# Optimization experiments

Hardware: AMD Instinct MI355X
Metric: run time of the kernel (lower is better)

The kernel has to match this reference:

```python
import jax, jax.numpy as jnp
import numpy as np
from jax import lax

TOP_K = 500
NEG_SLOPE = 0.01  # nn.LeakyReLU default
MASK_VAL = -10000.0


def setup_inputs() -> dict:
    key = jax.random.key(0)
    ks = jax.random.split(key, 6)
    B, N, D, H, C = 256, 131072, 2048, 512, 4096
    return {
        "inputs": jax.random.normal(ks[0], (B, D), dtype=jnp.float32),
        "targets": jax.random.randint(ks[1], (B,), 0, C, dtype=jnp.int32),
        "sample_features": jax.random.normal(ks[2], (N, D), dtype=jnp.float32),
        "sample_labels": jax.random.randint(ks[3], (N,), 0, C, dtype=jnp.int32),
        "fc1_w": jax.random.normal(ks[4], (D, H), dtype=jnp.float32) * (1.0 / np.sqrt(D)),
        "fc1_b": jnp.zeros((H,), dtype=jnp.float32),
        "fc2_w": jax.random.normal(ks[5], (H, 1), dtype=jnp.float32) * (1.0 / np.sqrt(H)),
        "fc2_b": jnp.zeros((1,), dtype=jnp.float32),
    }


def _head(d, w1, b1, w2, b2):
    h = jax.nn.leaky_relu(d @ w1 + b1, negative_slope=NEG_SLOPE)
    return h @ w2 + b2  # [B, 1] logits


def reference(inputs, targets, sample_features, sample_labels, fc1_w, fc1_b, fc2_w, fc2_b):
    B = inputs.shape[0]
    x = inputs / jnp.linalg.norm(inputs, axis=1, keepdims=True)  # F.normalize
    # similarities against memory bank: [B, N]
    sims = x @ sample_features.T
    pos_mask = sample_labels[None, :] == targets[:, None]  # [B, N]
    masked = jnp.where(pos_mask, MASK_VAL, sims)  # temp_sims[k, pos] = -10000
    # top-500 most-similar non-positive bank entries per row (sort()[1][-500:])
    _, top_idx = lax.top_k(masked, TOP_K)  # [B, 500]
    # stand-in for python random.choice (deterministic jax randomness)
    key = jax.random.key(42)
    k_neg, k_pos = jax.random.split(key)
    neg_pick = jax.random.randint(k_neg, (B,), 0, TOP_K)
    neg_sel = jnp.take_along_axis(top_idx, neg_pick[:, None], axis=1)[:, 0]  # [B]
    # uniform random positive via gumbel-argmax over the positive mask
    g = jax.random.gumbel(k_pos, pos_mask.shape, dtype=jnp.float32)
    pos_sel = jnp.argmax(jnp.where(pos_mask, g, -jnp.inf), axis=1)  # [B]
    x2_neg = sample_features[neg_sel]  # [B, D]
    x2_pos = sample_features[pos_sel]  # [B, D]
    logit_neg = _head(jnp.abs(x - x2_neg), fc1_w, fc1_b, fc2_w, fc2_b)
    logit_pos = _head(jnp.abs(x - x2_pos), fc1_w, fc1_b, fc2_w, fc2_b)
    # BCEWithLogits: y=1 -> softplus(-x); y=0 -> softplus(x); mean reduction
    loss_positive = jnp.mean(jax.nn.softplus(-logit_pos))
    loss_negtive = jnp.mean(jax.nn.softplus(logit_neg))
    loss_siamese = loss_positive + loss_negtive
    return loss_siamese
```

## Files before the change

kernel.cpp:

```cpp
#include <hip/hip_runtime.h>
#include <hip/hip_bf16.h>
#include <stdint.h>

#define N_BANK 131072
#define B_ROWS 256
#define DIM 2048
#define HID 512
#define CAND_CAP 1024
#define WIN 64
#define Z_THRESH 2.5528f

typedef __attribute__((ext_vector_type(8))) short bf16x8;
typedef __attribute__((ext_vector_type(8))) unsigned short ushort8;
typedef __attribute__((ext_vector_type(4))) float f32x4;

__device__ __forceinline__ void threefry2x32(uint32_t k0, uint32_t k1,
                                             uint32_t x0, uint32_t x1,
                                             uint32_t& o0, uint32_t& o1) {
  uint32_t ks0 = k0, ks1 = k1, ks2 = k0 ^ k1 ^ 0x1BD11BDAu;
  uint32_t ks[3] = {ks0, ks1, ks2};
  x0 += ks0; x1 += ks1;
  const int rotA[4] = {13, 15, 26, 6};
  const int rotB[4] = {17, 29, 16, 24};
  #pragma unroll
  for (int g = 0; g < 5; ++g) {
    const int* rr = (g & 1) ? rotB : rotA;
    #pragma unroll
    for (int i = 0; i < 4; ++i) {
      x0 += x1;
      x1 = (x1 << rr[i]) | (x1 >> (32 - rr[i]));
      x1 ^= x0;
    }
    x0 += ks[(g + 1) % 3];
    x1 += ks[(g + 2) % 3] + (uint32_t)(g + 1);
  }
  o0 = x0; o1 = x1;
}

__device__ __forceinline__ void jax_split(uint32_t k0, uint32_t k1,
                                          uint32_t& a0, uint32_t& a1,
                                          uint32_t& b0, uint32_t& b1) {
  uint32_t o00, o10, o01, o11;
  threefry2x32(k0, k1, 0u, 2u, o00, o10);
  threefry2x32(k0, k1, 1u, 3u, o01, o11);
  a0 = o00; a1 = o01;
  b0 = o10; b1 = o11;
}

__device__ __forceinline__ ushort f2bf(float f) {
  uint32_t u = __float_as_uint(f);
  return (ushort)((u + 0x7FFFu + ((u >> 16) & 1u)) >> 16);
}

__device__ __forceinline__ uint32_t cvt_pk(float lo, float hi) {
  uint32_t d;
  asm("v_cvt_pk_bf16_f32 %0, %1, %2" : "=v"(d) : "v"(lo), "v"(hi));
  return d;
}

__device__ __forceinline__ bf16x8 cvt8(float4 a, float4 b) {
  union { uint32_t u[4]; bf16x8 v; } r;
  r.u[0] = cvt_pk(a.x, a.y);
  r.u[1] = cvt_pk(a.z, a.w);
  r.u[2] = cvt_pk(b.x, b.y);
  r.u[3] = cvt_pk(b.z, b.w);
  return r.v;
}

__device__ __forceinline__ void async16(const void* g, void* l) {
  __builtin_amdgcn_global_load_lds((const __attribute__((address_space(1))) void*)g,
                                   (__attribute__((address_space(3))) void*)l, 16, 0, 0);
}

__global__ void zero_kernel(int* __restrict__ cand_cnt,
                            unsigned long long* __restrict__ pos_comb) {
  int t = threadIdx.x;
  cand_cnt[t] = 0;
  pos_comb[t] = 0ull;
}

__global__ __launch_bounds__(256) void prep_pos(const float* __restrict__ inputs,
                                                ushort* __restrict__ Abf,
                                                float* __restrict__ invn,
                                                float* __restrict__ thr,
                                                const int* __restrict__ labels,
                                                const int* __restrict__ targets,
                                                unsigned long long* __restrict__ pos_comb) {
  int bid = blockIdx.x, t = threadIdx.x;
  __shared__ int targ_s[256];
  __shared__ uint32_t bm[128];
  __shared__ double red[256];
  if (t < 128) bm[t] = 0u;
  int tg = targets[t];
  targ_s[t] = tg;

  double s = 0.0;
  if (bid < 256) {
    const float* src = inputs + (size_t)bid * DIM + t * 8;
    float4 v0 = *(const float4*)(src);
    float4 v1 = *(const float4*)(src + 4);
    s = (double)v0.x * v0.x + (double)v0.y * v0.y + (double)v0.z * v0.z + (double)v0.w * v0.w
      + (double)v1.x * v1.x + (double)v1.y * v1.y + (double)v1.z * v1.z + (double)v1.w * v1.w;
    ushort8 c = { f2bf(v0.x), f2bf(v0.y), f2bf(v0.z), f2bf(v0.w),
                  f2bf(v1.x), f2bf(v1.y), f2bf(v1.z), f2bf(v1.w) };
    int kt = t >> 3;
    int kk = (t >> 2) & 1;
    int lk = t & 3;
    int chunk = kt * 2048 + (bid >> 6) * 512 + kk * 256 + ((bid >> 4) & 3) * 64
              + lk * 16 + (bid & 15);
    *(ushort8*)(Abf + (size_t)chunk * 8) = c;
  }
  __syncthreads();
  atomicOr(&bm[tg >> 5], 1u << (tg & 31));
  __syncthreads();

  int n = bid * 256 + t;
  int c = labels[n];
  if ((bm[c >> 5] >> (c & 31)) & 1u) {
    uint32_t kn0, kn1, kp0, kp1;
    jax_split(0u, 42u, kn0, kn1, kp0, kp1);
    for (int r = 0; r < 256; ++r) {
      if (targ_s[r] == c) {
        uint32_t i = (uint32_t)r * (uint32_t)N_BANK + (uint32_t)n;
        uint32_t o0, o1, bits;
        if (i < (1u << 24)) { threefry2x32(kp0, kp1, i, i + (1u << 24), o0, o1); bits = o0; }
        else                { threefry2x32(kp0, kp1, i - (1u << 24), i, o0, o1); bits = o1; }
        unsigned long long comb =
            ((unsigned long long)((bits >> 9) + 1u) << 32) | (unsigned long long)(131071u - (uint32_t)n);
        atomicMax(&pos_comb[r], comb);
      }
    }
  }

  if (bid < 256) {
    red[t] = s;
    __syncthreads();
    for (int st = 128; st; st >>= 1) {
      if (t < st) red[t] += red[t + st];
      __syncthreads();
    }
    if (t == 0) {
      float nrm = sqrtf((float)red[0]);
      invn[bid] = 1.0f / nrm;
      thr[bid] = Z_THRESH * nrm;
    }
  }
}

#define STAGE(KTF, BUF)                                                       \
  {                                                                           \
    _Pragma("unroll")                                                         \
    for (int q = 0; q < 4; ++q) {                                             \
      int jj = wid * 4 + q;                                                   \
      int row_local = jj * 4 + (lane >> 4);                                   \
      int logc = (lane & 15) ^ (row_local & 15);                              \
      const float* g = F + (size_t)(bn + row_local) * DIM + (KTF) * 64 + logc * 4; \
      async16(g, (char*)(BUF) + jj * 1024);                                   \
    }                                                                         \
  }

#define LOADA(KT, DST)                                                        \
  {                                                                           \
    const ushort* ab = aptr + (size_t)(KT) * 16384;                           \
    _Pragma("unroll")                                                         \
    for (int q = 0; q < 8; ++q) DST[q] = *(const bf16x8*)(ab + q * 512);      \
  }

#define GMFMA(PR, AC)                                                         \
  {                                                                           \
    const float4* bp4 = (const float4*)(PR);                                  \
    _Pragma("unroll")                                                         \
    for (int kk = 0; kk < 2; ++kk) {                                          \
      bf16x8 bfv[4];                                                          \
      _Pragma("unroll")                                                       \
      for (int fj = 0; fj < 4; ++fj) {                                        \
        float4 x0 = bp4[(fj * 16 + lr) * 16 + ((kk * 8 + lk * 2) ^ lr)];      \
        float4 x1 = bp4[(fj * 16 + lr) * 16 + ((kk * 8 + lk * 2 + 1) ^ lr)];  \
        bfv[fj] = cvt8(x0, x1);                                               \
      }                                                                       \
      _Pragma("unroll")                                                       \
      for (int fi = 0; fi < 4; ++fi)                                          \
        _Pragma("unroll")                                                     \
        for (int fj = 0; fj < 4; ++fj)                                        \
          acc[fi][fj] = __builtin_amdgcn_mfma_f32_16x16x32_bf16(              \
              AC[kk * 4 + fi], bfv[fj], acc[fi][fj], 0, 0, 0);                \
    }                                                                         \
  }

#define SB() __builtin_amdgcn_sched_barrier(0)
#define WAITBAR(N) asm volatile("s_waitcnt vmcnt(" #N ")\n\ts_barrier" ::: "memory")
#define ROT4() { float* tt = p0; p0 = p1; p1 = p2; p2 = p3; p3 = tt; }

__global__ __launch_bounds__(256, 2) void gemm_select(
    const ushort* __restrict__ Abf, const float* __restrict__ F,
    const float* __restrict__ thr, const int* __restrict__ labels,
    const int* __restrict__ targets, float* __restrict__ cand_val,
    int* __restrict__ cand_idx, int* __restrict__ cand_cnt) {
  __shared__ __align__(16) float Bs32[4][64 * 64];
  const int tid = threadIdx.x;
  const int bn = blockIdx.x * 64;
  const int wid = tid >> 6;
  const int lane = tid & 63;
  const int lr = lane & 15;
  const int lk = lane >> 4;
  const ushort* aptr = Abf + (size_t)(wid * 512 + lane) * 8;

  f32x4 acc[4][4];
  #pragma unroll
  for (int i = 0; i < 4; ++i)
    #pragma unroll
    for (int j = 0; j < 4; ++j) acc[i][j] = (f32x4){0.f, 0.f, 0.f, 0.f};

  bf16x8 A0[8], A1[8];
  float* p0 = &Bs32[0][0];
  float* p1 = &Bs32[1][0];
  float* p2 = &Bs32[2][0];
  float* p3 = &Bs32[3][0];

  STAGE(0, p0);
  SB();
  LOADA(0, A0);
  SB();
  STAGE(1, p1);
  SB();
  STAGE(2, p2);
  WAITBAR(16);

  #pragma unroll 1
  for (int k2 = 0; k2 < 14; ++k2) {
    int kt = 2 * k2;
    LOADA(kt + 1, A1);
    SB();
    STAGE(kt + 3, p3);
    SB();
    GMFMA(p0, A0);
    WAITBAR(16);
    ROT4();
    LOADA(kt + 2, A0);
    SB();
    STAGE(kt + 4, p3);
    SB();
    GMFMA(p0, A1);
    WAITBAR(16);
    ROT4();
  }
  LOADA(29, A1);
  SB();
  STAGE(31, p3);
  SB();
  GMFMA(p0, A0);
  WAITBAR(16);
  ROT4();
  LOADA(30, A0);
  SB();
  GMFMA(p0, A1);
  WAITBAR(12);
  ROT4();
  LOADA(31, A1);
  SB();
  GMFMA(p0, A0);
  WAITBAR(8);
  ROT4();
  GMFMA(p0, A1);

  int lb[4];
  #pragma unroll
  for (int fj = 0; fj < 4; ++fj) lb[fj] = labels[bn + fj * 16 + lr];
  #pragma unroll
  for (int fi = 0; fi < 4; ++fi) {
    #pragma unroll
    for (int reg = 0; reg < 4; ++reg) {
      int row = wid * 64 + fi * 16 + lk * 4 + reg;
      float tr = thr[row];
      int tg = targets[row];
      #pragma unroll
      for (int fj = 0; fj < 4; ++fj) {
        float v = acc[fi][fj][reg];
        if (v > tr && lb[fj] != tg) {
          int p = atomicAdd(&cand_cnt[row], 1);
          if (p < CAND_CAP) {
            cand_val[row * CAND_CAP + p] = v;
            cand_idx[row * CAND_CAP + p] = bn + fj * 16 + lr;
          }
        }
      }
    }
  }
}

__global__ __launch_bounds__(512) void tail_kernel(const float* __restrict__ inputs,
                                                   const float* __restrict__ F,
                                                   const float* __restrict__ cand_val,
                                                   const int* __restrict__ cand_idx,
                                                   const int* __restrict__ cand_cnt,
                                                   const unsigned long long* __restrict__ pos_comb,
                                                   const float* __restrict__ invn,
                                                   float* __restrict__ Z) {
  int r = blockIdx.x;
  int tid = threadIdx.x;
  int m = cand_cnt[r]; if (m > CAND_CAP) m = CAND_CAP;
  __shared__ float vals[CAND_CAP];
  __shared__ int idxs[CAND_CAP];
  __shared__ float xr[DIM];
  __shared__ int wlist[WIN];
  __shared__ double dvals[WIN];
  __shared__ int wcnt, s_pick, s_neg;

  if (tid == 0) {
    wcnt = 0; s_neg = 0;
    uint32_t kn0, kn1, kp0, kp1, k10, k11, k20, k21, o0, o1, hi, lo;
    jax_split(0u, 42u, kn0, kn1, kp0, kp1);
    jax_split(kn0, kn1, k10, k11, k20, k21);
    if (r < 128) { threefry2x32(k10, k11, (uint32_t)r, (uint32_t)(r + 128), o0, o1); hi = o0; }
    else         { threefry2x32(k10, k11, (uint32_t)(r - 128), (uint32_t)r, o0, o1); hi = o1; }
    if (r < 128) { threefry2x32(k20, k21, (uint32_t)r, (uint32_t)(r + 128), o0, o1); lo = o0; }
    else         { threefry2x32(k20, k21, (uint32_t)(r - 128), (uint32_t)r, o0, o1); lo = o1; }
    s_pick = (int)(((hi % 500u) * 296u + (lo % 500u)) % 500u);
  }
  for (int d = tid; d < DIM; d += 512) xr[d] = inputs[(size_t)r * DIM + d];
  for (int c = tid; c < m; c += 512) {
    vals[c] = cand_val[r * CAND_CAP + c];
    idxs[c] = cand_idx[r * CAND_CAP + c];
  }
  __syncthreads();
  int pick = s_pick;
  int lo = pick - 32; if (lo < 0) lo = 0;
  int hi = pick + 32; if (hi > m) hi = m;
  for (int c = tid; c < m; c += 512) {
    float v = vals[c]; int id = idxs[c]; int rk = 0;
    for (int j = 0; j < m; ++j) {
      float vj = vals[j];
      rk += (vj > v) || (vj == v && idxs[j] < id);
    }
    if (rk >= lo && rk < hi) { int p = atomicAdd(&wcnt, 1); if (p < WIN) wlist[p] = c; }
  }
  __syncthreads();
  int wn = wcnt; if (wn > WIN) wn = WIN;
  int wave = tid >> 6, lane = tid & 63;
  for (int w = wave; w < wn; w += 8) {
    const float* f = F + (size_t)idxs[wlist[w]] * DIM;
    double s = 0.0;
    for (int d = lane; d < DIM; d += 64) s += (double)xr[d] * (double)f[d];
    for (int off = 32; off; off >>= 1) s += __shfl_down(s, off);
    if (lane == 0) dvals[w] = s;
  }
  __syncthreads();
  if (tid < wn) {
    double v = dvals[tid]; int id = idxs[wlist[tid]]; int rk = lo;
    for (int j = 0; j < wn; ++j) {
      double vj = dvals[j];
      rk += (vj > v) || (vj == v && idxs[wlist[j]] < id);
    }
    if (rk == pick) s_neg = id;
  }
  __syncthreads();

  unsigned long long pc = pos_comb[r];
  int sp = pc ? (int)(131071u - (uint32_t)(pc & 0xffffffffull)) : 0;
  int sn = s_neg;
  float inv = invn[r];
  const float* fp = F + (size_t)sp * DIM;
  const float* fn = F + (size_t)sn * DIM;
  float* zp = Z + (size_t)(2 * r) * DIM;
  float* zn = Z + (size_t)(2 * r + 1) * DIM;
  for (int d = tid; d < DIM; d += 512) {
    float x = xr[d] * inv;
    zp[d] = fabsf(x - fp[d]);
    zn[d] = fabsf(x - fn[d]);
  }
}

__global__ __launch_bounds__(256) void head_gemm(const float* __restrict__ Z,
                                                 const float* __restrict__ W1,
                                                 const float* __restrict__ b1,
                                                 const float* __restrict__ W2,
                                                 float* __restrict__ partials) {
  __shared__ float As[32][68];
  __shared__ float Ws[32][68];
  __shared__ float part[64][17];
  const int bj = blockIdx.x;
  const int bi = blockIdx.y;
  const int tid = threadIdx.x;
  const int tx = tid & 15, ty = tid >> 4;
  const int zr0 = bi * 64, j0 = bj * 64;
  float acc[4][4] = {};

  const int zrow = tid >> 2, kz0 = (tid & 3) * 8;
  const int dd = tid >> 3, jj0 = (tid & 7) * 8;
  for (int kt = 0; kt < 64; ++kt) {
    float4 za = *(const float4*)(Z + (size_t)(zr0 + zrow) * DIM + kt * 32 + kz0);
    float4 zb = *(const float4*)(Z + (size_t)(zr0 + zrow) * DIM + kt * 32 + kz0 + 4);
    float4 wa = *(const float4*)(W1 + (size_t)(kt * 32 + dd) * HID + j0 + jj0);
    float4 wb = *(const float4*)(W1 + (size_t)(kt * 32 + dd) * HID + j0 + jj0 + 4);
    __syncthreads();
    As[kz0 + 0][zrow] = za.x; As[kz0 + 1][zrow] = za.y;
    As[kz0 + 2][zrow] = za.z; As[kz0 + 3][zrow] = za.w;
    As[kz0 + 4][zrow] = zb.x; As[kz0 + 5][zrow] = zb.y;
    As[kz0 + 6][zrow] = zb.z; As[kz0 + 7][zrow] = zb.w;
    *(float4*)(&Ws[dd][jj0]) = wa;
    *(float4*)(&Ws[dd][jj0 + 4]) = wb;
    __syncthreads();
    #pragma unroll
    for (int kk = 0; kk < 32; ++kk) {
      float a[4], w[4];
      *(float4*)a = *(const float4*)(&As[kk][ty * 4]);
      *(float4*)w = *(const float4*)(&Ws[kk][tx * 4]);
      #pragma unroll
      for (int i = 0; i < 4; ++i)
        #pragma unroll
        for (int j = 0; j < 4; ++j)
          acc[i][j] = fmaf(a[i], w[j], acc[i][j]);
    }
  }
  float psum[4] = {0.f, 0.f, 0.f, 0.f};
  #pragma unroll
  for (int j = 0; j < 4; ++j) {
    int jj = j0 + tx * 4 + j;
    float b = b1[jj], w2 = W2[jj];
    #pragma unroll
    for (int i = 0; i < 4; ++i) {
      float h = acc[i][j] + b;
      h = h >= 0.f ? h : 0.01f * h;
      psum[i] = fmaf(h, w2, psum[i]);
    }
  }
  #pragma unroll
  for (int i = 0; i < 4; ++i) part[ty * 4 + i][tx] = psum[i];
  __syncthreads();
  if (tid < 64) {
    float s = 0.f;
    #pragma unroll
    for (int x = 0; x < 16; ++x) s += part[tid][x];
    partials[(size_t)(zr0 + tid) * 8 + bj] = s;
  }
}

__global__ __launch_bounds__(512) void final_kernel(const float* __restrict__ partials,
                                                    const float* __restrict__ b2,
                                                    float* __restrict__ out) {
  __shared__ float red[512];
  int zr = threadIdx.x;
  float lg = b2[0];
  for (int bj = 0; bj < 8; ++bj) lg += partials[(size_t)zr * 8 + bj];
  float x = (zr & 1) ? lg : -lg;
  float sp = fmaxf(x, 0.f) + log1pf(expf(-fabsf(x)));
  red[zr] = sp * (1.0f / 256.0f);
  __syncthreads();
  for (int st = 256; st; st >>= 1) {
    if (zr < st) red[zr] += red[zr + st];
    __syncthreads();
  }
  if (zr == 0) out[0] = red[0];
}

extern "C" void kernel_launch(void* const* d_in, const int* in_sizes, int n_in,
                              void* d_out, int out_size, void* d_ws, size_t ws_size,
                              hipStream_t stream) {
  (void)in_sizes; (void)n_in; (void)out_size; (void)ws_size;
  const float* inputs = (const float*)d_in[0];
  const int* targets  = (const int*)d_in[1];
  const float* F      = (const float*)d_in[2];
  const int* labels   = (const int*)d_in[3];
  const float* W1     = (const float*)d_in[4];
  const float* b1     = (const float*)d_in[5];
  const float* W2     = (const float*)d_in[6];
  const float* b2     = (const float*)d_in[7];
  float* out = (float*)d_out;

  char* ws = (char*)d_ws;
  size_t off = 0;
  ushort* Abf     = (ushort*)(ws + off); off += (size_t)B_ROWS * DIM * 2;
  float* cand_val = (float*)(ws + off); off += (size_t)B_ROWS * CAND_CAP * 4;
  int* cand_idx   = (int*)(ws + off);   off += (size_t)B_ROWS * CAND_CAP * 4;
  int* cand_cnt   = (int*)(ws + off);   off += 1024;
  unsigned long long* pos_comb = (unsigned long long*)(ws + off); off += 2048;
  float* invn     = (float*)(ws + off); off += 1024;
  float* thr      = (float*)(ws + off); off += 1024;
  float* partials = (float*)(ws + off); off += 512 * 8 * 4;
  off = (off + 255) & ~(size_t)255;
  float* Z        = (float*)(ws + off); off += (size_t)512 * DIM * 4;

  zero_kernel<<<1, 256, 0, stream>>>(cand_cnt, pos_comb);
  prep_pos<<<512, 256, 0, stream>>>(inputs, Abf, invn, thr, labels, targets, pos_comb);
  gemm_select<<<N_BANK / 64, 256, 0, stream>>>(Abf, F, thr, labels, targets,
                                               cand_val, cand_idx, cand_cnt);
  tail_kernel<<<B_ROWS, 512, 0, stream>>>(inputs, F, cand_val, cand_idx, cand_cnt,
                                          pos_comb, invn, Z);
  head_gemm<<<dim3(8, 8), 256, 0, stream>>>(Z, W1, b1, W2, partials);
  final_kernel<<<1, 512, 0, stream>>>(partials, b2, out);
}
```

Measured before the change: 688.8 us.

## Stage bank tiles via registers with bf16 conversion before LDS, double-buffered

Replaces the async global-to-LDS fp32 staging of bank-feature tiles (four fp32 buffers) with register loads that are converted to bf16 once per element and written into two bf16 LDS buffers. This removes the redundant per-wave fp32-to-bf16 conversion in the MFMA inner loop and halves LDS traffic and footprint. In exchange, global loads now pass through VGPRs, which raises register pressure, and the prefetch depth drops from three tiles to two.

Measured after the change: 631.5 us. 8.3% less time.

```diff
diff --git a/kernel.cpp b/kernel.cpp
--- a/kernel.cpp
+++ b/kernel.cpp
@@ -58,18 +58,13 @@
   return d;
 }
 
-__device__ __forceinline__ bf16x8 cvt8(float4 a, float4 b) {
-  union { uint32_t u[4]; bf16x8 v; } r;
+__device__ __forceinline__ ushort8 cvt8u(float4 a, float4 b) {
+  union { uint32_t u[4]; ushort8 v; } r;
   r.u[0] = cvt_pk(a.x, a.y);
   r.u[1] = cvt_pk(a.z, a.w);
   r.u[2] = cvt_pk(b.x, b.y);
   r.u[3] = cvt_pk(b.z, b.w);
   return r.v;
-}
-
-__device__ __forceinline__ void async16(const void* g, void* l) {
-  __builtin_amdgcn_global_load_lds((const __attribute__((address_space(1))) void*)g,
-                                   (__attribute__((address_space(3))) void*)l, 16, 0, 0);
 }
 
 __global__ void zero_kernel(int* __restrict__ cand_cnt,
@@ -147,18 +142,6 @@
   }
 }
 
-#define STAGE(KTF, BUF)                                                       \
-  {                                                                           \
-    _Pragma("unroll")                                                         \
-    for (int q = 0; q < 4; ++q) {                                             \
-      int jj = wid * 4 + q;                                                   \
-      int row_local = jj * 4 + (lane >> 4);                                   \
-      int logc = (lane & 15) ^ (row_local & 15);                              \
-      const float* g = F + (size_t)(bn + row_local) * DIM + (KTF) * 64 + logc * 4; \
-      async16(g, (char*)(BUF) + jj * 1024);                                   \
-    }                                                                         \
-  }
-
 #define LOADA(KT, DST)                                                        \
   {                                                                           \
     const ushort* ab = aptr + (size_t)(KT) * 16384;                           \
@@ -166,18 +149,15 @@
     for (int q = 0; q < 8; ++q) DST[q] = *(const bf16x8*)(ab + q * 512);      \
   }
 
-#define GMFMA(PR, AC)                                                         \
+#define GMFMA(CUR, AC)                                                        \
   {                                                                           \
-    const float4* bp4 = (const float4*)(PR);                                  \
     _Pragma("unroll")                                                         \
     for (int kk = 0; kk < 2; ++kk) {                                          \
       bf16x8 bfv[4];                                                          \
       _Pragma("unroll")                                                       \
-      for (int fj = 0; fj < 4; ++fj) {                                        \
-        float4 x0 = bp4[(fj * 16 + lr) * 16 + ((kk * 8 + lk * 2) ^ lr)];      \
-        float4 x1 = bp4[(fj * 16 + lr) * 16 + ((kk * 8 + lk * 2 + 1) ^ lr)];  \
-        bfv[fj] = cvt8(x0, x1);                                               \
-      }                                                                       \
+      for (int fj = 0; fj < 4; ++fj)                                          \
+        bfv[fj] = *(const bf16x8*)(&Bs[CUR][(fj * 16 + lr) * 64 +             \
+                        (((kk * 4 + lk) ^ (lr & 7)) * 8)]);                   \
       _Pragma("unroll")                                                       \
       for (int fi = 0; fi < 4; ++fi)                                          \
         _Pragma("unroll")                                                     \
@@ -188,21 +168,47 @@
   }
 
 #define SB() __builtin_amdgcn_sched_barrier(0)
-#define WAITBAR(N) asm volatile("s_waitcnt vmcnt(" #N ")\n\ts_barrier" ::: "memory")
-#define ROT4() { float* tt = p0; p0 = p1; p1 = p2; p2 = p3; p3 = tt; }
+
+#define GSTEP(KT, AC, AN, FISS, FCVT, CUR, NXT, DOA, DOF)                     \
+  {                                                                           \
+    if (DOA) { LOADA((KT) + 1, AN); }                                         \
+    SB();                                                                     \
+    if (DOF) {                                                                \
+      const float* fp2 = fptr + ((KT) + 2) * 64;                              \
+      FISS[0] = *(const float4*)(fp2);                                        \
+      FISS[1] = *(const float4*)(fp2 + 4);                                    \
+      FISS[2] = *(const float4*)(fp2 + 8);                                    \
+      FISS[3] = *(const float4*)(fp2 + 12);                                   \
+    }                                                                         \
+    SB();                                                                     \
+    GMFMA(CUR, AC);                                                           \
+    if ((KT) < 31) {                                                          \
+      *(ushort8*)(&Bs[NXT][bo0]) = cvt8u(FCVT[0], FCVT[1]);                   \
+      *(ushort8*)(&Bs[NXT][bo1]) = cvt8u(FCVT[2], FCVT[3]);                   \
+      asm volatile("s_waitcnt lgkmcnt(0)\n\ts_barrier" ::: "memory");         \
+    }                                                                         \
+  }
 
 __global__ __launch_bounds__(256, 2) void gemm_select(
     const ushort* __restrict__ Abf, const float* __restrict__ F,
     const float* __restrict__ thr, const int* __restrict__ labels,
     const int* __restrict__ targets, float* __restrict__ cand_val,
     int* __restrict__ cand_idx, int* __restrict__ cand_cnt) {
-  __shared__ __align__(16) float Bs32[4][64 * 64];
+  __shared__ ushort Bs[2][64 * 64];
   const int tid = threadIdx.x;
   const int bn = blockIdx.x * 64;
   const int wid = tid >> 6;
   const int lane = tid & 63;
   const int lr = lane & 15;
   const int lk = lane >> 4;
+
+  const int frow = tid >> 2;
+  const int fq = tid & 3;
+  const float* fptr = F + (size_t)(bn + frow) * DIM + fq * 16;
+  const int fr7 = frow & 7;
+  const int bo0 = frow * 64 + ((fq * 2) ^ fr7) * 8;
+  const int bo1 = frow * 64 + ((fq * 2 + 1) ^ fr7) * 8;
+
   const ushort* aptr = Abf + (size_t)(wid * 512 + lane) * 8;
 
   f32x4 acc[4][4];
@@ -212,56 +218,33 @@
     for (int j = 0; j < 4; ++j) acc[i][j] = (f32x4){0.f, 0.f, 0.f, 0.f};
 
   bf16x8 A0[8], A1[8];
-  float* p0 = &Bs32[0][0];
-  float* p1 = &Bs32[1][0];
-  float* p2 = &Bs32[2][0];
-  float* p3 = &Bs32[3][0];
-
-  STAGE(0, p0);
-  SB();
+  float4 fE[4], fO[4];
+
   LOADA(0, A0);
   SB();
-  STAGE(1, p1);
+  fE[0] = *(const float4*)(fptr);
+  fE[1] = *(const float4*)(fptr + 4);
+  fE[2] = *(const float4*)(fptr + 8);
+  fE[3] = *(const float4*)(fptr + 12);
+  fO[0] = *(const float4*)(fptr + 64);
+  fO[1] = *(const float4*)(fptr + 68);
+  fO[2] = *(const float4*)(fptr + 72);
+  fO[3] = *(const float4*)(fptr + 76);
   SB();
-  STAGE(2, p2);
-  WAITBAR(16);
+  *(ushort8*)(&Bs[0][bo0]) = cvt8u(fE[0], fE[1]);
+  *(ushort8*)(&Bs[0][bo1]) = cvt8u(fE[2], fE[3]);
+  asm volatile("s_waitcnt lgkmcnt(0)\n\ts_barrier" ::: "memory");
 
   #pragma unroll 1
   for (int k2 = 0; k2 < 14; ++k2) {
     int kt = 2 * k2;
-    LOADA(kt + 1, A1);
-    SB();
-    STAGE(kt + 3, p3);
-    SB();
-    GMFMA(p0, A0);
-    WAITBAR(16);
-    ROT4();
-    LOADA(kt + 2, A0);
-    SB();
-    STAGE(kt + 4, p3);
-    SB();
-    GMFMA(p0, A1);
-    WAITBAR(16);
-    ROT4();
-  }
-  LOADA(29, A1);
-  SB();
-  STAGE(31, p3);
-  SB();
-  GMFMA(p0, A0);
-  WAITBAR(16);
-  ROT4();
-  LOADA(30, A0);
-  SB();
-  GMFMA(p0, A1);
-  WAITBAR(12);
-  ROT4();
-  LOADA(31, A1);
-  SB();
-  GMFMA(p0, A0);
-  WAITBAR(8);
-  ROT4();
-  GMFMA(p0, A1);
+    GSTEP(kt,       A0, A1, fE, fO, 0, 1, 1, 1);
+    GSTEP((kt + 1), A1, A0, fO, fE, 1, 0, 1, 1);
+  }
+  GSTEP(28, A0, A1, fE, fO, 0, 1, 1, 1);
+  GSTEP(29, A1, A0, fO, fE, 1, 0, 1, 1);
+  GSTEP(30, A0, A1, fE, fO, 0, 1, 1, 0);
+  GSTEP(31, A1, A0, fO, fE, 1, 0, 0, 0);
 
   int lb[4];
   #pragma unroll
```
